# Kernel optimization log

Measured on AMD Instinct MI355X. Metric: run time of the kernel, lower is better.

Reference implementation:

```python
import jax, jax.numpy as jnp
import numpy as np

# YOLOv1 loss constants (match init_kwargs)
S, B, C = 14, 2, 20
LAMBDA_COORD, LAMBDA_NOOBJ = 5.0, 0.5
BATCH = 4096


def setup_inputs() -> dict:
    key = jax.random.key(0)
    k1, k2, k3, k4, k5 = jax.random.split(key, 5)
    N = 5 * B + C
    # predictions must be positive (torch.sqrt on w,h)
    pred = jax.random.uniform(k1, (BATCH, S, S, N), jnp.float32, 1e-3, 1.0)
    # build target exactly like convert_to_yolo_format: obj cells carry the
    # same (x,y,w,h,1) in every one of the B box slots + one-hot class;
    # empty cells are all zeros (so target[...,4]==0 is the noobj mask).
    obj = (jax.random.uniform(k2, (BATCH, S, S)) < 0.3).astype(jnp.float32)
    xy = jax.random.uniform(k3, (BATCH, S, S, 2))            # cell-relative center
    wh = jax.random.uniform(k4, (BATCH, S, S, 2), minval=0.05, maxval=0.95)
    box = jnp.concatenate([xy, wh, obj[..., None]], -1) * obj[..., None]  # [Bt,S,S,5]
    boxes = jnp.tile(box, (1, 1, 1, B))                       # [Bt,S,S,5B]
    labels = jax.random.randint(k5, (BATCH, S, S), 0, C)
    cls = jax.nn.one_hot(labels, C, dtype=jnp.float32) * obj[..., None]
    target = jnp.concatenate([boxes, cls], -1)                # [Bt,S,S,5B+C]
    return {"pred": pred, "target": target}


def _to_xyxy(box):
    # torch: xyxy[:, :2] = xy/S - 0.5*wh ; xyxy[:, 2:4] = xy/S + 0.5*wh
    c = box[..., :2] / S
    h = 0.5 * box[..., 2:4]
    return jnp.concatenate([c - h, c + h], -1)


def _yolo_loss(pred, target):
    bs = pred.shape[0]
    obj = target[..., 4] > 0                                  # [Bt,S,S] coord_mask
    pb = pred[..., :5 * B].reshape(pred.shape[:-1] + (B, 5))  # [Bt,S,S,B,5]
    tb = target[..., :5 * B].reshape(target.shape[:-1] + (B, 5))
    t0 = tb[..., 0, :]                                        # torch uses bbox_target[i] (first box)

    # IoU of each of the B predicted boxes against the cell's target box
    p4 = _to_xyxy(pb)                                         # [Bt,S,S,B,4]
    t4 = _to_xyxy(t0)[..., None, :]                           # [Bt,S,S,1,4]
    lt = jnp.maximum(p4[..., :2], t4[..., :2])
    rb = jnp.minimum(p4[..., 2:], t4[..., 2:])
    whi = jnp.clip(rb - lt, 0.0)
    inter = whi[..., 0] * whi[..., 1]
    area_p = (p4[..., 2] - p4[..., 0]) * (p4[..., 3] - p4[..., 1])
    area_t = (t4[..., 2] - t4[..., 0]) * (t4[..., 3] - t4[..., 1])
    # torch stores max_iou via .item() -> detached constant target
    iou = jax.lax.stop_gradient(inter / (area_p + area_t - inter))  # [Bt,S,S,B]
    max_iou = iou.max(-1)
    idx = iou.argmax(-1)
    resp = (idx[..., None] == jnp.arange(B)) & obj[..., None]       # responsible box mask

    rf = resp.astype(pred.dtype)
    of = obj.astype(pred.dtype)
    nf = 1.0 - of

    # coord losses (responsible boxes only)
    loss_xy = jnp.sum(rf[..., None] * (pb[..., :2] - tb[..., :2]) ** 2)
    pwh = jnp.where(resp[..., None], pb[..., 2:4], 1.0)  # safe sqrt outside mask
    twh = jnp.where(resp[..., None], tb[..., 2:4], 1.0)
    loss_wh = jnp.sum(rf[..., None] * (jnp.sqrt(pwh) - jnp.sqrt(twh)) ** 2)
    # objectness: pred conf vs (detached) max IoU
    loss_obj = jnp.sum(rf * (pb[..., 4] - max_iou[..., None]) ** 2)
    # no-object: conf channels of every box slot in empty cells
    loss_noobj = jnp.sum(nf[..., None] * (pb[..., 4] - tb[..., 4]) ** 2)
    # class loss over object cells
    loss_cls = jnp.sum(of[..., None] * (pred[..., 5 * B:] - target[..., 5 * B:]) ** 2)

    loss = (LAMBDA_COORD * (loss_xy + loss_wh) + loss_obj
            + LAMBDA_NOOBJ * loss_noobj + loss_cls) / bs
    return loss


def reference(pred, target):
    return _yolo_loss(pred, target)
```

## Files before the change

### kernel.cpp

```cpp
#include <hip/hip_runtime.h>


typedef __attribute__((address_space(3))) void*       as3_void;
typedef const __attribute__((address_space(1))) void* as1_cvoid;

static __device__ __forceinline__ void gl_lds16(const float* g, float* l) {
    __builtin_amdgcn_global_load_lds((as1_cvoid)g, (as3_void)l, 16, 0, 0);
}
static __device__ __forceinline__ void gl_lds4(const float* g, float* l) {
    __builtin_amdgcn_global_load_lds((as1_cvoid)g, (as3_void)l, 4, 0, 0);
}

__global__ __launch_bounds__(256) void yolo_loss_kernel(
    const float* __restrict__ pred, const float* __restrict__ target,
    float* __restrict__ partials)
{
    __shared__ float sp[4][1920];
    __shared__ float st[4][1920];

    const int lane = threadIdx.x & 63;
    const int wid  = threadIdx.x >> 6;
    const size_t tile0 = ((size_t)blockIdx.x * 4 + wid) * 64;
    const float* gp = pred   + tile0 * 30;
    const float* gt = target + tile0 * 30;
    float* swp = sp[wid];
    float* swt = st[wid];

    #pragma unroll
    for (int i = 0; i < 7; ++i)
        gl_lds16(gp + i*256 + lane*4, swp + i*256);
    gl_lds4(gp + 1792 + lane, swp + 1792);
    gl_lds4(gp + 1856 + lane, swp + 1856);
    #pragma unroll
    for (int i = 0; i < 7; ++i)
        gl_lds16(gt + i*256 + lane*4, swt + i*256);
    gl_lds4(gt + 1792 + lane, swt + 1792);
    gl_lds4(gt + 1856 + lane, swt + 1856);

    __builtin_amdgcn_s_waitcnt(0);

    float pv[30];
    {
        const float2* rp = (const float2*)&swp[lane * 30];
        #pragma unroll
        for (int j = 0; j < 15; ++j) {
            float2 a = rp[j]; pv[2*j] = a.x; pv[2*j+1] = a.y;
        }
    }

    float t0, t1, t2v, t3, t4;
    float tcls[20];
    {
        const float* tb = &swt[lane * 30];
        float2 a = *(const float2*)(tb + 0);
        float2 b = *(const float2*)(tb + 2);
        t0 = a.x; t1 = a.y; t2v = b.x; t3 = b.y;
        t4 = tb[4];
        const float2* tc = (const float2*)(tb + 10);
        #pragma unroll
        for (int j = 0; j < 10; ++j) {
            float2 c = tc[j]; tcls[2*j] = c.x; tcls[2*j+1] = c.y;
        }
    }

    const float invS = 1.0f / 14.0f;
    const bool obj = t4 > 0.0f;

    float tcx = t0 * invS, tcy = t1 * invS;
    float thw = 0.5f * t2v, thh = 0.5f * t3;
    float tx1 = tcx - thw, ty1 = tcy - thh;
    float tx2 = tcx + thw, ty2 = tcy + thh;
    float area_t = (tx2 - tx1) * (ty2 - ty1);

    float iou0 = 0.0f, iou1 = 0.0f;
    #pragma unroll
    for (int b = 0; b < 2; ++b) {
        float cx = pv[5*b + 0] * invS, cy = pv[5*b + 1] * invS;
        float hw = 0.5f * pv[5*b + 2], hh = 0.5f * pv[5*b + 3];
        float x1 = cx - hw, y1 = cy - hh, x2 = cx + hw, y2 = cy + hh;
        float lx = fmaxf(x1, tx1), ly = fmaxf(y1, ty1);
        float rx = fminf(x2, tx2), ry = fminf(y2, ty2);
        float w = fmaxf(rx - lx, 0.0f), h = fmaxf(ry - ly, 0.0f);
        float inter = w * h;
        float area_p = (x2 - x1) * (y2 - y1);
        float iou = inter / (area_p + area_t - inter);
        if (b == 0) iou0 = iou; else iou1 = iou;
    }
    const bool  sel     = iou1 > iou0;
    const float max_iou = fmaxf(iou0, iou1);

    float local;
    if (obj) {
        float pbx = sel ? pv[5] : pv[0];
        float pby = sel ? pv[6] : pv[1];
        float pbw = sel ? pv[7] : pv[2];
        float pbh = sel ? pv[8] : pv[3];
        float pbc = sel ? pv[9] : pv[4];

        float dx = pbx - t0, dy = pby - t1;
        float loss_xy = dx*dx + dy*dy;

        float sws = sqrtf(pbw) - sqrtf(t2v);
        float shs = sqrtf(pbh) - sqrtf(t3);
        float loss_wh = sws*sws + shs*shs;

        float dob = pbc - max_iou;
        float loss_obj = dob * dob;

        float loss_cls = 0.0f;
        #pragma unroll
        for (int c = 0; c < 20; ++c) {
            float d = pv[10 + c] - tcls[c];
            loss_cls = fmaf(d, d, loss_cls);
        }
        local = 5.0f * (loss_xy + loss_wh) + loss_obj + loss_cls;
    } else {
        float d0 = pv[4] - t4;
        float d1 = pv[9] - t4;
        local = 0.5f * (d0*d0 + d1*d1);
    }

    #pragma unroll
    for (int off = 32; off > 0; off >>= 1)
        local += __shfl_down(local, off, 64);

    __shared__ float wsum[4];
    if (lane == 0) wsum[wid] = local;
    __syncthreads();
    if (threadIdx.x == 0)
        partials[blockIdx.x] = wsum[0] + wsum[1] + wsum[2] + wsum[3];
}

__global__ __launch_bounds__(256) void reduce_kernel(
    const float* __restrict__ partials, float* __restrict__ out, int n)
{
    float local = 0.0f;
    for (int i = threadIdx.x; i < n; i += 256)
        local += partials[i];

    #pragma unroll
    for (int off = 32; off > 0; off >>= 1)
        local += __shfl_down(local, off, 64);

    __shared__ float wsum[4];
    const int lane = threadIdx.x & 63;
    const int wid  = threadIdx.x >> 6;
    if (lane == 0) wsum[wid] = local;
    __syncthreads();
    if (threadIdx.x == 0)
        out[0] = (wsum[0] + wsum[1] + wsum[2] + wsum[3]) * (1.0f / 4096.0f);
}

extern "C" void kernel_launch(void* const* d_in, const int* in_sizes, int n_in,
                              void* d_out, int out_size, void* d_ws, size_t ws_size,
                              hipStream_t stream) {
    const float* pred   = (const float*)d_in[0];
    const float* target = (const float*)d_in[1];
    float* out      = (float*)d_out;
    float* partials = (float*)d_ws;

    yolo_loss_kernel<<<3136, 256, 0, stream>>>(pred, target, partials);
    reduce_kernel<<<1, 256, 0, stream>>>(partials, out, 3136);
}
```

Baseline: 202.1 us.

## Make loss kernel persistent with double-buffered async LDS prefetch of tiles

Replaces the one-tile-per-wave grid of 3136 blocks with 256 persistent blocks whose waves walk tiles with stride 1024. Each wave prefetches the next tile into a second LDS buffer via global_load_lds while it computes the current one, using a partial vmcnt wait. This is meant to hide memory latency and cut launch and reduction overhead. The cost is LDS doubling to about 120KB per block, which limits occupancy to one block per CU. The fixed 256-block grid may also underfill a 256-CU device's bandwidth.

```diff
diff --git a/kernel.cpp b/kernel.cpp
--- a/kernel.cpp
+++ b/kernel.cpp
@@ -11,121 +11,146 @@
     __builtin_amdgcn_global_load_lds((as1_cvoid)g, (as3_void)l, 4, 0, 0);
 }
 
+#define NTILES 12544
+#define WSTRIDE 1024
+
+#define WAITCNT_VM18 (2 | (7<<4) | (15<<8) | (1<<14))
+#define WAITCNT_VM0  (0 | (7<<4) | (15<<8))
+
 __global__ __launch_bounds__(256) void yolo_loss_kernel(
     const float* __restrict__ pred, const float* __restrict__ target,
     float* __restrict__ partials)
 {
-    __shared__ float sp[4][1920];
-    __shared__ float st[4][1920];
+    __shared__ float stage[4][2][3840];
 
     const int lane = threadIdx.x & 63;
     const int wid  = threadIdx.x >> 6;
-    const size_t tile0 = ((size_t)blockIdx.x * 4 + wid) * 64;
-    const float* gp = pred   + tile0 * 30;
-    const float* gt = target + tile0 * 30;
-    float* swp = sp[wid];
-    float* swt = st[wid];
+    const int wgid = blockIdx.x * 4 + wid;
 
-    #pragma unroll
-    for (int i = 0; i < 7; ++i)
-        gl_lds16(gp + i*256 + lane*4, swp + i*256);
-    gl_lds4(gp + 1792 + lane, swp + 1792);
-    gl_lds4(gp + 1856 + lane, swp + 1856);
-    #pragma unroll
-    for (int i = 0; i < 7; ++i)
-        gl_lds16(gt + i*256 + lane*4, swt + i*256);
-    gl_lds4(gt + 1792 + lane, swt + 1792);
-    gl_lds4(gt + 1856 + lane, swt + 1856);
+    auto stage_tile = [&](int t, float* dst) {
+        const float* gp = pred   + (size_t)t * 1920;
+        const float* gt = target + (size_t)t * 1920;
+        float* dp = dst;
+        float* dt = dst + 1920;
+        #pragma unroll
+        for (int i = 0; i < 7; ++i) gl_lds16(gp + i*256 + lane*4, dp + i*256);
+        gl_lds4(gp + 1792 + lane, dp + 1792);
+        gl_lds4(gp + 1856 + lane, dp + 1856);
+        #pragma unroll
+        for (int i = 0; i < 7; ++i) gl_lds16(gt + i*256 + lane*4, dt + i*256);
+        gl_lds4(gt + 1792 + lane, dt + 1792);
+        gl_lds4(gt + 1856 + lane, dt + 1856);
+    };
 
-    __builtin_amdgcn_s_waitcnt(0);
+    float acc = 0.0f;
+    int ph = 0;
+    int t = wgid;
+    stage_tile(t, stage[wid][0]);
 
-    float pv[30];
-    {
-        const float2* rp = (const float2*)&swp[lane * 30];
+    while (t < NTILES) {
+        const int nxt = t + WSTRIDE;
+        const bool pre = (nxt < NTILES);
+        if (pre) {
+            stage_tile(nxt, stage[wid][ph ^ 1]);
+            __builtin_amdgcn_s_waitcnt(WAITCNT_VM18);
+        } else {
+            __builtin_amdgcn_s_waitcnt(WAITCNT_VM0);
+        }
+
+        const float* swp = stage[wid][ph];
+        const float* swt = swp + 1920;
+
+        float pv[30];
+        {
+            const float2* rp = (const float2*)&swp[lane * 30];
+            #pragma unroll
+            for (int j = 0; j < 15; ++j) {
+                float2 a = rp[j]; pv[2*j] = a.x; pv[2*j+1] = a.y;
+            }
+        }
+        float t0, t1, t2v, t3, t4;
+        float tcls[20];
+        {
+            const float* tb = &swt[lane * 30];
+            float2 a = *(const float2*)(tb + 0);
+            float2 b = *(const float2*)(tb + 2);
+            t0 = a.x; t1 = a.y; t2v = b.x; t3 = b.y;
+            t4 = tb[4];
+            const float2* tc = (const float2*)(tb + 10);
+            #pragma unroll
+            for (int j = 0; j < 10; ++j) {
+                float2 c = tc[j]; tcls[2*j] = c.x; tcls[2*j+1] = c.y;
+            }
+        }
+
+        const float invS = 1.0f / 14.0f;
+        const bool obj = t4 > 0.0f;
+
+        float tcx = t0 * invS, tcy = t1 * invS;
+        float thw = 0.5f * t2v, thh = 0.5f * t3;
+        float tx1 = tcx - thw, ty1 = tcy - thh;
+        float tx2 = tcx + thw, ty2 = tcy + thh;
+        float area_t = (tx2 - tx1) * (ty2 - ty1);
+
+        float iou0 = 0.0f, iou1 = 0.0f;
         #pragma unroll
-        for (int j = 0; j < 15; ++j) {
-            float2 a = rp[j]; pv[2*j] = a.x; pv[2*j+1] = a.y;
+        for (int b = 0; b < 2; ++b) {
+            float cx = pv[5*b + 0] * invS, cy = pv[5*b + 1] * invS;
+            float hw = 0.5f * pv[5*b + 2], hh = 0.5f * pv[5*b + 3];
+            float x1 = cx - hw, y1 = cy - hh, x2 = cx + hw, y2 = cy + hh;
+            float lx = fmaxf(x1, tx1), ly = fmaxf(y1, ty1);
+            float rx = fminf(x2, tx2), ry = fminf(y2, ty2);
+            float w = fmaxf(rx - lx, 0.0f), h = fmaxf(ry - ly, 0.0f);
+            float inter = w * h;
+            float area_p = (x2 - x1) * (y2 - y1);
+            float iou = inter / (area_p + area_t - inter);
+            if (b == 0) iou0 = iou; else iou1 = iou;
         }
-    }
+        const bool  sel     = iou1 > iou0;
+        const float max_iou = fmaxf(iou0, iou1);
 
-    float t0, t1, t2v, t3, t4;
-    float tcls[20];
-    {
-        const float* tb = &swt[lane * 30];
-        float2 a = *(const float2*)(tb + 0);
-        float2 b = *(const float2*)(tb + 2);
-        t0 = a.x; t1 = a.y; t2v = b.x; t3 = b.y;
-        t4 = tb[4];
-        const float2* tc = (const float2*)(tb + 10);
-        #pragma unroll
-        for (int j = 0; j < 10; ++j) {
-            float2 c = tc[j]; tcls[2*j] = c.x; tcls[2*j+1] = c.y;
+        float local;
+        if (obj) {
+            float pbx = sel ? pv[5] : pv[0];
+            float pby = sel ? pv[6] : pv[1];
+            float pbw = sel ? pv[7] : pv[2];
+            float pbh = sel ? pv[8] : pv[3];
+            float pbc = sel ? pv[9] : pv[4];
+
+            float dx = pbx - t0, dy = pby - t1;
+            float loss_xy = dx*dx + dy*dy;
+
+            float sws = sqrtf(pbw) - sqrtf(t2v);
+            float shs = sqrtf(pbh) - sqrtf(t3);
+            float loss_wh = sws*sws + shs*shs;
+
+            float dob = pbc - max_iou;
+            float loss_obj = dob * dob;
+
+            float loss_cls = 0.0f;
+            #pragma unroll
+            for (int c = 0; c < 20; ++c) {
+                float d = pv[10 + c] - tcls[c];
+                loss_cls = fmaf(d, d, loss_cls);
+            }
+            local = 5.0f * (loss_xy + loss_wh) + loss_obj + loss_cls;
+        } else {
+            float d0 = pv[4] - t4;
+            float d1 = pv[9] - t4;
+            local = 0.5f * (d0*d0 + d1*d1);
         }
-    }
+        acc += local;
 
-    const float invS = 1.0f / 14.0f;
-    const bool obj = t4 > 0.0f;
-
-    float tcx = t0 * invS, tcy = t1 * invS;
-    float thw = 0.5f * t2v, thh = 0.5f * t3;
-    float tx1 = tcx - thw, ty1 = tcy - thh;
-    float tx2 = tcx + thw, ty2 = tcy + thh;
-    float area_t = (tx2 - tx1) * (ty2 - ty1);
-
-    float iou0 = 0.0f, iou1 = 0.0f;
-    #pragma unroll
-    for (int b = 0; b < 2; ++b) {
-        float cx = pv[5*b + 0] * invS, cy = pv[5*b + 1] * invS;
-        float hw = 0.5f * pv[5*b + 2], hh = 0.5f * pv[5*b + 3];
-        float x1 = cx - hw, y1 = cy - hh, x2 = cx + hw, y2 = cy + hh;
-        float lx = fmaxf(x1, tx1), ly = fmaxf(y1, ty1);
-        float rx = fminf(x2, tx2), ry = fminf(y2, ty2);
-        float w = fmaxf(rx - lx, 0.0f), h = fmaxf(ry - ly, 0.0f);
-        float inter = w * h;
-        float area_p = (x2 - x1) * (y2 - y1);
-        float iou = inter / (area_p + area_t - inter);
-        if (b == 0) iou0 = iou; else iou1 = iou;
-    }
-    const bool  sel     = iou1 > iou0;
-    const float max_iou = fmaxf(iou0, iou1);
-
-    float local;
-    if (obj) {
-        float pbx = sel ? pv[5] : pv[0];
-        float pby = sel ? pv[6] : pv[1];
-        float pbw = sel ? pv[7] : pv[2];
-        float pbh = sel ? pv[8] : pv[3];
-        float pbc = sel ? pv[9] : pv[4];
-
-        float dx = pbx - t0, dy = pby - t1;
-        float loss_xy = dx*dx + dy*dy;
-
-        float sws = sqrtf(pbw) - sqrtf(t2v);
-        float shs = sqrtf(pbh) - sqrtf(t3);
-        float loss_wh = sws*sws + shs*shs;
-
-        float dob = pbc - max_iou;
-        float loss_obj = dob * dob;
-
-        float loss_cls = 0.0f;
-        #pragma unroll
-        for (int c = 0; c < 20; ++c) {
-            float d = pv[10 + c] - tcls[c];
-            loss_cls = fmaf(d, d, loss_cls);
-        }
-        local = 5.0f * (loss_xy + loss_wh) + loss_obj + loss_cls;
-    } else {
-        float d0 = pv[4] - t4;
-        float d1 = pv[9] - t4;
-        local = 0.5f * (d0*d0 + d1*d1);
+        ph ^= 1;
+        t = nxt;
     }
 
     #pragma unroll
     for (int off = 32; off > 0; off >>= 1)
-        local += __shfl_down(local, off, 64);
+        acc += __shfl_down(acc, off, 64);
 
     __shared__ float wsum[4];
-    if (lane == 0) wsum[wid] = local;
+    if (lane == 0) wsum[wid] = acc;
     __syncthreads();
     if (threadIdx.x == 0)
         partials[blockIdx.x] = wsum[0] + wsum[1] + wsum[2] + wsum[3];
@@ -159,6 +184,6 @@
     float* out      = (float*)d_out;
     float* partials = (float*)d_ws;
 
-    yolo_loss_kernel<<<3136, 256, 0, stream>>>(pred, target, partials);
-    reduce_kernel<<<1, 256, 0, stream>>>(partials, out, 3136);
+    yolo_loss_kernel<<<256, 256, 0, stream>>>(pred, target, partials);
+    reduce_kernel<<<1, 256, 0, stream>>>(partials, out, 256);
 }
```

Result: slower. 206.5 us (+2.2%).
